# Kernel tuning notes

Hardware: AMD Instinct MI355X
Metric: run time of the kernel (lower is better)

The kernel has to match this reference:

```python
import jax, jax.numpy as jnp
import numpy as np

N = 100000   # nodes
E = 1600000  # edges (before self-loops)
F_IN = 128
H = 64
G = 512      # graphs in batch


def _add_self_loops(edge_index, n):
    loop = jnp.arange(n, dtype=edge_index.dtype)
    src = jnp.concatenate([edge_index[0], loop])
    dst = jnp.concatenate([edge_index[1], loop])
    return src, dst


def _gcn_norm(src, dst, n):
    # PyG GCNConv: deg over targets with self-loops, norm = d^-1/2[src]*d^-1/2[dst]
    deg = jax.ops.segment_sum(jnp.ones_like(dst, dtype=jnp.float32), dst, num_segments=n)
    dinv = jnp.where(deg > 0, jax.lax.rsqrt(deg), 0.0)
    return dinv[src] * dinv[dst]


def _gcn_conv(x, src, dst, norm, W, b):
    xw = x @ W                                # [N, H]
    msg = xw[src] * norm[:, None]             # [E+N, H] gather + scale
    out = jax.ops.segment_sum(msg, dst, num_segments=x.shape[0])
    return out + b


def setup_inputs() -> dict:
    key = jax.random.key(0)
    ks = jax.random.split(key, 9)
    x = jax.random.normal(ks[0], (N, F_IN), dtype=jnp.float32)
    edge_index = jax.random.randint(ks[1], (2, E), 0, N, dtype=jnp.int32)
    batch = jnp.sort(jax.random.randint(ks[2], (N,), 0, G, dtype=jnp.int32))
    s1 = 1.0 / np.sqrt(F_IN)
    s2 = 1.0 / np.sqrt(H)
    W1 = jax.random.uniform(ks[3], (F_IN, H), jnp.float32, -s1, s1)
    b1 = jnp.zeros((H,), jnp.float32)
    W2 = jax.random.uniform(ks[4], (H, H), jnp.float32, -s2, s2)
    b2 = jnp.zeros((H,), jnp.float32)
    Wl = jax.random.uniform(ks[5], (H, 1), jnp.float32, -s2, s2)
    bl = jnp.zeros((1,), jnp.float32)
    return {"x": x, "edge_index": edge_index, "batch": batch,
            "W1": W1, "b1": b1, "W2": W2, "b2": b2, "Wl": Wl, "bl": bl}


def reference(x, edge_index, batch, W1, b1, W2, b2, Wl, bl):
    n = x.shape[0]
    src, dst = _add_self_loops(edge_index, n)
    norm = _gcn_norm(src, dst, n)
    h = jax.nn.relu(_gcn_conv(x, src, dst, norm, W1, b1))
    h = jax.nn.relu(_gcn_conv(h, src, dst, norm, W2, b2))
    # global mean pool over graphs
    sums = jax.ops.segment_sum(h, batch, num_segments=G)          # [G, H]
    cnt = jax.ops.segment_sum(jnp.ones((n,), jnp.float32), batch, num_segments=G)
    pooled = sums / jnp.maximum(cnt, 1.0)[:, None]
    return jax.nn.sigmoid(pooled @ Wl + bl)                        # [G, 1]
```

## Files before the change

kernel.cpp:

```cpp
#include <hip/hip_runtime.h>
#include <hip/hip_bf16.h>
#include <cmath>

#define F_IN 128
#define HDIM 64
#define NPB 128
#define NB1 512
#define CAP 2560

typedef __attribute__((ext_vector_type(8))) short bf16x8;
typedef __attribute__((ext_vector_type(4))) float f32x4;
typedef __attribute__((ext_vector_type(2))) float f32x2;

__device__ __forceinline__ float bf2f(unsigned short u) {
    union { unsigned int i; float f; } v; v.i = ((unsigned int)u) << 16; return v.f;
}
__device__ __forceinline__ unsigned short f2bf(float f) {
    __hip_bfloat16 h = __float2bfloat16(f);
    union { __hip_bfloat16 h; unsigned short u; } c; c.h = h; return c.u;
}
__device__ __forceinline__ unsigned char f2fp8(float f) {
    int p = __builtin_amdgcn_cvt_pk_fp8_f32(f, f, 0, false);
    return (unsigned char)(p & 0xff);
}
__device__ __forceinline__ void fp8x8_acc(uint2 v, float* a) {
    f32x2 f;
    f = __builtin_amdgcn_cvt_pk_f32_fp8(v.x, false); a[0] += f.x; a[1] += f.y;
    f = __builtin_amdgcn_cvt_pk_f32_fp8(v.x, true);  a[2] += f.x; a[3] += f.y;
    f = __builtin_amdgcn_cvt_pk_f32_fp8(v.y, false); a[4] += f.x; a[5] += f.y;
    f = __builtin_amdgcn_cvt_pk_f32_fp8(v.y, true);  a[6] += f.x; a[7] += f.y;
}


__launch_bounds__(256)
__global__ void p0_count(const int* __restrict__ dst, int* __restrict__ blk_cnt,
                         int E, int nbuk, int chunk,
                         const float* __restrict__ W1, const float* __restrict__ W2,
                         unsigned short* __restrict__ w1t, unsigned short* __restrict__ w2t) {
    int tid = threadIdx.x;
    if (blockIdx.x >= NB1) {
        int t = (blockIdx.x - NB1) * 256 + tid;
        if (t < F_IN * 64) {
            int c = t & 63, k = t >> 6;
            w1t[c * F_IN + k] = f2bf(W1[t]);
        } else if (t < F_IN * 64 + HDIM * 64) {
            int u = t - F_IN * 64;
            int c = u & 63, k = u >> 6;
            w2t[c * HDIM + k] = f2bf(W2[u]);
        }
        return;
    }
    __shared__ int hist[1024];
    for (int i = tid; i < nbuk; i += 256) hist[i] = 0;
    __syncthreads();
    int lo = blockIdx.x * chunk;
    int hi = min(E, lo + chunk);
    for (int e = lo + tid; e < hi; e += 256)
        atomicAdd(&hist[dst[e] >> 7], 1);
    __syncthreads();
    for (int i = tid; i < nbuk; i += 256)
        blk_cnt[i * NB1 + blockIdx.x] = hist[i];
}


__launch_bounds__(256)
__global__ void p_scan_blocks(int* __restrict__ blk_cnt, int* __restrict__ bucket_cnt,
                              int nbuk, const int* __restrict__ batch,
                              int* __restrict__ gstart, int n, int G) {
    int tid = threadIdx.x;
    if (blockIdx.x >= nbuk) {
        int g = (blockIdx.x - nbuk) * 256 + tid;
        if (g > G) return;
        int lo = 0, hi = n;
        while (lo < hi) {
            int mid = (lo + hi) >> 1;
            if (batch[mid] < g) lo = mid + 1; else hi = mid;
        }
        gstart[g] = lo;
        return;
    }
    __shared__ int sd[256];
    int b = blockIdx.x;
    int2* row = (int2*)(blk_cnt + (size_t)b * NB1);
    int2 v = row[tid];
    int s0 = v.x, s1 = s0 + v.y;
    sd[tid] = s1;
    __syncthreads();
    for (int off = 1; off < 256; off <<= 1) {
        int a = (tid >= off) ? sd[tid - off] : 0;
        __syncthreads();
        sd[tid] += a;
        __syncthreads();
    }
    int base = sd[tid] - s1;
    row[tid] = make_int2(base, base + s0);
    if (tid == 255) bucket_cnt[b] = sd[255];
}


__launch_bounds__(256)
__global__ void p1_place(const int* __restrict__ src, const int* __restrict__ dst,
                         const int* __restrict__ blk_cnt, int* __restrict__ pairs,
                         int E, int nbuk, int chunk) {
    __shared__ int cur[1024];
    int tid = threadIdx.x;
    for (int i = tid; i < nbuk; i += 256)
        cur[i] = i * CAP + blk_cnt[i * NB1 + blockIdx.x];
    __syncthreads();
    int lo = blockIdx.x * chunk;
    int hi = min(E, lo + chunk);
    for (int e = lo + tid; e < hi; e += 256) {
        int d = dst[e];
        int pos = atomicAdd(&cur[d >> 7], 1);
        pairs[pos] = (src[e] << 7) | (d & 127);
    }
}


__launch_bounds__(256)
__global__ void p2_csr(const int* __restrict__ pairs, const int* __restrict__ bucket_cnt,
                       float* __restrict__ dinv, int* __restrict__ col,
                       int4* __restrict__ slot_hdr, int n) {
    __shared__ int dl[128];
    __shared__ int sc[128];
    __shared__ int cur[128];
    __shared__ int h64[64];
    __shared__ int s64[64];
    int b = blockIdx.x, tid = threadIdx.x;
    int nlo = b << 7;
    int eb = b * CAP;
    int ee = eb + bucket_cnt[b];
    if (tid < 128) dl[tid] = 0;
    if (tid < 64) h64[tid] = 0;
    __syncthreads();
    for (int e = eb + tid; e < ee; e += 256)
        atomicAdd(&dl[pairs[e] & 127], 1);
    __syncthreads();
    int d0 = 0, excl = 0;
    if (tid < 128) {
        d0 = dl[tid];
        sc[tid] = d0;
    }
    __syncthreads();
    for (int off = 1; off < 128; off <<= 1) {
        int a = (tid >= off && tid < 128) ? sc[tid - off] : 0;
        __syncthreads();
        if (tid < 128) sc[tid] += a;
        __syncthreads();
    }
    if (tid < 128) {
        excl = sc[tid] - d0;
        int node = nlo + tid;
        float dv = rsqrtf((float)(d0 + 1));
        if (node < n) dinv[node] = dv;
        cur[tid] = eb + excl;
        int bin = min(d0, 63);
        atomicAdd(&h64[bin], 1);
    }
    __syncthreads();
    if (tid == 0) { int run = 0; for (int i = 0; i < 64; ++i) { s64[i] = run; run += h64[i]; } }
    __syncthreads();
    if (tid < 64) h64[tid] = 0;
    __syncthreads();
    if (tid < 128) {
        int node = nlo + tid;
        int bin = min(d0, 63);
        int pos = s64[bin] + atomicAdd(&h64[bin], 1);
        float dv = rsqrtf((float)(d0 + 1));
        int4 hdr;
        hdr.x = (node < n) ? node : 0x7fffffff;
        hdr.y = eb + excl;
        hdr.z = d0;
        hdr.w = __float_as_int(dv);
        slot_hdr[nlo + pos] = hdr;
    }
    __syncthreads();
    for (int e = eb + tid; e < ee; e += 256) {
        unsigned int v = (unsigned int)pairs[e];
        int p = atomicAdd(&cur[v & 127], 1);
        col[p] = (int)(v >> 7);
    }
}


template <int K>
__launch_bounds__(256)
__global__ void matmul_mfma(const float* __restrict__ X, const unsigned short* __restrict__ Wt,
                            const float* __restrict__ dinv, unsigned char* __restrict__ out,
                            int n) {
    constexpr int KS  = K / 32;
    constexpr int LDX = K + 8;
    __shared__ unsigned short Xs[64 * LDX];
    __shared__ unsigned short Ws[64 * LDX];

    int tid = threadIdx.x;
    int rowbase = blockIdx.x * 64;

    for (int i = tid; i < 64 * (K / 8); i += 256) {
        int r = i / (K / 8), ch = i % (K / 8);
        *(bf16x8*)(Ws + r * LDX + ch * 8) = ((const bf16x8*)Wt)[i];
    }
    {
        const float4* X4 = (const float4*)X;
        for (int i = tid; i < 64 * (K / 4); i += 256) {
            int r = i / (K / 4), k4 = i % (K / 4);
            ushort4 u = { 0, 0, 0, 0 };
            int gr = rowbase + r;
            if (gr < n) {
                float4 v = X4[(size_t)gr * (K / 4) + k4];
                u.x = f2bf(v.x); u.y = f2bf(v.y); u.z = f2bf(v.z); u.w = f2bf(v.w);
            }
            *(ushort4*)(Xs + r * LDX + k4 * 4) = u;
        }
    }
    __syncthreads();

    int wave = tid >> 6, lane = tid & 63;
    int q = lane >> 4, nn = lane & 15;

    f32x4 acc[4] = {{0,0,0,0},{0,0,0,0},{0,0,0,0},{0,0,0,0}};
    int mrow = wave * 16 + nn;
#pragma unroll
    for (int s = 0; s < KS; ++s) {
        bf16x8 af = *(const bf16x8*)(Xs + mrow * LDX + s * 32 + q * 8);
#pragma unroll
        for (int c = 0; c < 4; ++c) {
            bf16x8 bf = *(const bf16x8*)(Ws + (c * 16 + nn) * LDX + s * 32 + q * 8);
            acc[c] = __builtin_amdgcn_mfma_f32_16x16x32_bf16(af, bf, acc[c], 0, 0, 0);
        }
    }

#pragma unroll
    for (int r = 0; r < 4; ++r) {
        int row = rowbase + wave * 16 + q * 4 + r;
        if (row >= n) continue;
        float dv = dinv[row];
#pragma unroll
        for (int c = 0; c < 4; ++c)
            out[(size_t)row * HDIM + c * 16 + nn] = f2fp8(acc[c][r] * dv);
    }
}


__launch_bounds__(256)
__global__ void matmul_mfma_b16(const unsigned short* __restrict__ X,
                                const unsigned short* __restrict__ Wt,
                                const float* __restrict__ dinv, unsigned char* __restrict__ out,
                                int n) {
    constexpr int K = 64, KS = 2, LDX = K + 8;
    __shared__ unsigned short Xs[64 * LDX];
    __shared__ unsigned short Ws[64 * LDX];

    int tid = threadIdx.x;
    int rowbase = blockIdx.x * 64;

    for (int i = tid; i < 64 * (K / 8); i += 256) {
        int r = i / (K / 8), ch = i % (K / 8);
        *(bf16x8*)(Ws + r * LDX + ch * 8) = ((const bf16x8*)Wt)[i];
    }
    for (int i = tid; i < 64 * 8; i += 256) {
        int r = i >> 3, c = i & 7;
        int gr = rowbase + r;
        bf16x8 u;
        if (gr < n) u = ((const bf16x8*)X)[(size_t)gr * 8 + c];
        else { short z[8] = {0,0,0,0,0,0,0,0}; u = *(bf16x8*)z; }
        *(bf16x8*)(Xs + r * LDX + c * 8) = u;
    }
    __syncthreads();

    int wave = tid >> 6, lane = tid & 63;
    int q = lane >> 4, nn = lane & 15;

    f32x4 acc[4] = {{0,0,0,0},{0,0,0,0},{0,0,0,0},{0,0,0,0}};
    int mrow = wave * 16 + nn;
#pragma unroll
    for (int s = 0; s < KS; ++s) {
        bf16x8 af = *(const bf16x8*)(Xs + mrow * LDX + s * 32 + q * 8);
#pragma unroll
        for (int c = 0; c < 4; ++c) {
            bf16x8 bf = *(const bf16x8*)(Ws + (c * 16 + nn) * LDX + s * 32 + q * 8);
            acc[c] = __builtin_amdgcn_mfma_f32_16x16x32_bf16(af, bf, acc[c], 0, 0, 0);
        }
    }

#pragma unroll
    for (int r = 0; r < 4; ++r) {
        int row = rowbase + wave * 16 + q * 4 + r;
        if (row >= n) continue;
        float dv = dinv[row];
#pragma unroll
        for (int c = 0; c < 4; ++c)
            out[(size_t)row * HDIM + c * 16 + nn] = f2fp8(acc[c][r] * dv);
    }
}


__launch_bounds__(256)
__global__ void csr_gather8_fp8(const int4* __restrict__ slot_hdr, const int* __restrict__ col,
                                const uint2* __restrict__ xws, const float* __restrict__ bias,
                                bf16x8* __restrict__ outb, int nslots, int n) {
    int t = blockIdx.x * 256 + threadIdx.x;
    int slot = t >> 3;
    if (slot >= nslots) return;
    int L = t & 7;
    int4 hdr = slot_hdr[slot];
    int node = hdr.x;
    if (node >= n) return;
    int s = hdr.y;
    int end = s + hdr.z;
    float dv = __int_as_float(hdr.w);

    float a[8] = {0, 0, 0, 0, 0, 0, 0, 0};
    fp8x8_acc(xws[(size_t)node * 8 + L], a);

    int e = s;
    for (; e + 8 <= end; e += 8) {
        uint2 v0 = xws[(size_t)col[e + 0] * 8 + L];
        uint2 v1 = xws[(size_t)col[e + 1] * 8 + L];
        uint2 v2 = xws[(size_t)col[e + 2] * 8 + L];
        uint2 v3 = xws[(size_t)col[e + 3] * 8 + L];
        uint2 v4 = xws[(size_t)col[e + 4] * 8 + L];
        uint2 v5 = xws[(size_t)col[e + 5] * 8 + L];
        uint2 v6 = xws[(size_t)col[e + 6] * 8 + L];
        uint2 v7 = xws[(size_t)col[e + 7] * 8 + L];
        fp8x8_acc(v0, a); fp8x8_acc(v1, a); fp8x8_acc(v2, a); fp8x8_acc(v3, a);
        fp8x8_acc(v4, a); fp8x8_acc(v5, a); fp8x8_acc(v6, a); fp8x8_acc(v7, a);
    }
    for (; e + 4 <= end; e += 4) {
        uint2 v0 = xws[(size_t)col[e + 0] * 8 + L];
        uint2 v1 = xws[(size_t)col[e + 1] * 8 + L];
        uint2 v2 = xws[(size_t)col[e + 2] * 8 + L];
        uint2 v3 = xws[(size_t)col[e + 3] * 8 + L];
        fp8x8_acc(v0, a); fp8x8_acc(v1, a); fp8x8_acc(v2, a); fp8x8_acc(v3, a);
    }
    for (; e < end; ++e)
        fp8x8_acc(xws[(size_t)col[e] * 8 + L], a);

    int f0 = L * 8;
    bf16x8 o;
#pragma unroll
    for (int j = 0; j < 8; ++j)
        o[j] = (short)f2bf(fmaxf(fmaf(a[j], dv, bias[f0 + j]), 0.0f));
    outb[(size_t)node * 8 + L] = o;
}


__launch_bounds__(256)
__global__ void pool_head(const unsigned short* __restrict__ h, const int* __restrict__ gstart,
                          const float* __restrict__ Wl, const float* __restrict__ bl,
                          float* __restrict__ out, int G) {
    int g = blockIdx.x;
    int s = gstart[g], e = gstart[g + 1];
    int f  = threadIdx.x & 63;
    int rg = threadIdx.x >> 6;
    float acc = 0.0f;
    for (int i = s + rg; i < e; i += 4)
        acc += bf2f(h[(size_t)i * HDIM + f]);
    __shared__ float red[4][HDIM];
    red[rg][f] = acc;
    __syncthreads();
    if (rg == 0) {
        float v = (red[0][f] + red[1][f]) + (red[2][f] + red[3][f]);
        float c = fmaxf((float)(e - s), 1.0f);
        v = v * Wl[f] * (1.0f / c);
#pragma unroll
        for (int off = 32; off; off >>= 1) v += __shfl_down(v, off, 64);
        if (f == 0) out[g] = 1.0f / (1.0f + expf(-(v + bl[0])));
    }
}


extern "C" void kernel_launch(void* const* d_in, const int* in_sizes, int n_in,
                              void* d_out, int out_size, void* d_ws, size_t ws_size,
                              hipStream_t stream) {
    const float* x   = (const float*)d_in[0];
    const int* ei    = (const int*)d_in[1];
    const int* batch = (const int*)d_in[2];
    const float* W1  = (const float*)d_in[3];
    const float* b1  = (const float*)d_in[4];
    const float* W2  = (const float*)d_in[5];
    const float* b2  = (const float*)d_in[6];
    const float* Wl  = (const float*)d_in[7];
    const float* bl  = (const float*)d_in[8];
    float* out = (float*)d_out;

    const int n = in_sizes[0] / F_IN;
    const int E = in_sizes[1] / 2;
    const int G = out_size;

    const int* srcp = ei;
    const int* dstp = ei + E;

    int nbuk = (n + NPB - 1) / NPB;
    int nslots = nbuk * NPB;

    char* wsb = (char*)d_ws;
    auto alloc = [&](size_t bytes) { char* p = wsb; wsb += (bytes + 255) & ~(size_t)255; return p; };
    float* dinv       = (float*)alloc((size_t)n * 4);
    int4*  slot_hdr   = (int4*)alloc((size_t)nslots * 16);
    int*   bucket_cnt = (int*)alloc(1024 * 4);
    int*   blk_cnt    = (int*)alloc((size_t)nbuk * NB1 * 4);
    int*   pairs      = (int*)alloc((size_t)nbuk * CAP * 4);
    int*   colx       = (int*)alloc((size_t)nbuk * CAP * 4);
    unsigned short* w1t  = (unsigned short*)alloc((size_t)F_IN * HDIM * 2);
    unsigned short* w2t  = (unsigned short*)alloc((size_t)HDIM * HDIM * 2);
    unsigned char*  xws8 = (unsigned char*)alloc((size_t)n * HDIM);
    unsigned short* xh1  = (unsigned short*)alloc((size_t)n * HDIM * 2);
    unsigned short* xh2  = (unsigned short*)alloc((size_t)n * HDIM * 2);
    int*   gstart     = (int*)alloc(((size_t)G + 1) * 4);

    const int TB = 256;
    int gMM  = (n + 63) / 64;
    int chunk = (E + NB1 - 1) / NB1;
    int gG8  = (nslots * 8 + TB - 1) / TB;

    p0_count<<<NB1 + 48, TB, 0, stream>>>(dstp, blk_cnt, E, nbuk, chunk, W1, W2, w1t, w2t);
    p_scan_blocks<<<nbuk + 3, TB, 0, stream>>>(blk_cnt, bucket_cnt, nbuk, batch, gstart, n, G);
    p1_place<<<NB1, TB, 0, stream>>>(srcp, dstp, blk_cnt, pairs, E, nbuk, chunk);
    p2_csr<<<nbuk, TB, 0, stream>>>(pairs, bucket_cnt, dinv, colx, slot_hdr, n);

    matmul_mfma<F_IN><<<gMM, 256, 0, stream>>>(x, w1t, dinv, xws8, n);
    csr_gather8_fp8<<<gG8, TB, 0, stream>>>(slot_hdr, colx, (const uint2*)xws8,
                                            b1, (bf16x8*)xh1, nslots, n);

    matmul_mfma_b16<<<gMM, 256, 0, stream>>>(xh1, w2t, dinv, xws8, n);
    csr_gather8_fp8<<<gG8, TB, 0, stream>>>(slot_hdr, colx, (const uint2*)xws8,
                                            b2, (bf16x8*)xh2, nslots, n);

    pool_head<<<G, 256, 0, stream>>>(xh2, gstart, Wl, bl, out, G);
}
```

Before: 243.4 us.

## Fuse layer-1 matmul into front kernel and apply dinv per edge in gather

The first X@W1 matmul moves into the front count kernel so it no longer waits on degree normalization and runs concurrently with histogram counting. It stores unscaled fp8 XW1, and the first gather kernel multiplies each neighbour by dinv[src] loaded per edge. This removes one kernel launch and a serial dependency, at the cost of an extra random dinv load and multiply per edge in layer 1. W1 is transposed and converted per tile instead of once, and fp8 quantization now happens before scaling.

```diff
diff --git a/kernel.cpp b/kernel.cpp
--- a/kernel.cpp
+++ b/kernel.cpp
@@ -22,6 +22,13 @@
 __device__ __forceinline__ unsigned char f2fp8(float f) {
     int p = __builtin_amdgcn_cvt_pk_fp8_f32(f, f, 0, false);
     return (unsigned char)(p & 0xff);
+}
+__device__ __forceinline__ void fp8x8_fma(uint2 v, float s, float* a) {
+    f32x2 f;
+    f = __builtin_amdgcn_cvt_pk_f32_fp8(v.x, false); a[0] += s * f.x; a[1] += s * f.y;
+    f = __builtin_amdgcn_cvt_pk_f32_fp8(v.x, true);  a[2] += s * f.x; a[3] += s * f.y;
+    f = __builtin_amdgcn_cvt_pk_f32_fp8(v.y, false); a[4] += s * f.x; a[5] += s * f.y;
+    f = __builtin_amdgcn_cvt_pk_f32_fp8(v.y, true);  a[6] += s * f.x; a[7] += s * f.y;
 }
 __device__ __forceinline__ void fp8x8_acc(uint2 v, float* a) {
     f32x2 f;
@@ -33,43 +40,79 @@
 
 
 __launch_bounds__(256)
-__global__ void p0_count(const int* __restrict__ dst, int* __restrict__ blk_cnt,
-                         int E, int nbuk, int chunk,
-                         const float* __restrict__ W1, const float* __restrict__ W2,
-                         unsigned short* __restrict__ w1t, unsigned short* __restrict__ w2t) {
-    int tid = threadIdx.x;
-    if (blockIdx.x >= NB1) {
-        int t = (blockIdx.x - NB1) * 256 + tid;
-        if (t < F_IN * 64) {
-            int c = t & 63, k = t >> 6;
-            w1t[c * F_IN + k] = f2bf(W1[t]);
-        } else if (t < F_IN * 64 + HDIM * 64) {
-            int u = t - F_IN * 64;
-            int c = u & 63, k = u >> 6;
-            w2t[c * HDIM + k] = f2bf(W2[u]);
-        }
+__global__ void fused_front(const int* __restrict__ dst, int* __restrict__ blk_cnt,
+                            int E, int nbuk, int chunk,
+                            const float* __restrict__ X, const float* __restrict__ W1,
+                            unsigned char* __restrict__ xws8, int ntiles, int n,
+                            const float* __restrict__ W2, unsigned short* __restrict__ w2t,
+                            const int* __restrict__ batch, int* __restrict__ gstart, int G) {
+    __shared__ __align__(16) char SMEM[34816];
+    int tid = threadIdx.x, bid = blockIdx.x;
+
+    if (bid < NB1) {
+        int* hist = (int*)SMEM;
+        for (int i = tid; i < nbuk; i += 256) hist[i] = 0;
+        __syncthreads();
+        int lo = bid * chunk, hi = min(E, lo + chunk);
+        for (int e = lo + tid; e < hi; e += 256)
+            atomicAdd(&hist[dst[e] >> 7], 1);
+        __syncthreads();
+        for (int i = tid; i < nbuk; i += 256)
+            blk_cnt[(size_t)i * NB1 + bid] = hist[i];
         return;
     }
-    __shared__ int hist[1024];
-    for (int i = tid; i < nbuk; i += 256) hist[i] = 0;
-    __syncthreads();
-    int lo = blockIdx.x * chunk;
-    int hi = min(E, lo + chunk);
-    for (int e = lo + tid; e < hi; e += 256)
-        atomicAdd(&hist[dst[e] >> 7], 1);
-    __syncthreads();
-    for (int i = tid; i < nbuk; i += 256)
-        blk_cnt[i * NB1 + blockIdx.x] = hist[i];
-}
-
-
-__launch_bounds__(256)
-__global__ void p_scan_blocks(int* __restrict__ blk_cnt, int* __restrict__ bucket_cnt,
-                              int nbuk, const int* __restrict__ batch,
-                              int* __restrict__ gstart, int n, int G) {
-    int tid = threadIdx.x;
-    if (blockIdx.x >= nbuk) {
-        int g = (blockIdx.x - nbuk) * 256 + tid;
+    if (bid < NB1 + ntiles) {
+        constexpr int K = F_IN, KS = K / 32, LDX = K + 8;
+        unsigned short* Xs = (unsigned short*)SMEM;
+        unsigned short* Ws = (unsigned short*)(SMEM + 64 * LDX * 2);
+        int rowbase = (bid - NB1) * 64;
+        for (int i = tid; i < K * 64; i += 256) {
+            int k = i >> 6, c = i & 63;
+            Ws[c * LDX + k] = f2bf(W1[i]);
+        }
+        const float4* X4 = (const float4*)X;
+        for (int i = tid; i < 64 * (K / 4); i += 256) {
+            int r = i / (K / 4), k4 = i % (K / 4);
+            ushort4 u = { 0, 0, 0, 0 };
+            int gr = rowbase + r;
+            if (gr < n) {
+                float4 v = X4[(size_t)gr * (K / 4) + k4];
+                u.x = f2bf(v.x); u.y = f2bf(v.y); u.z = f2bf(v.z); u.w = f2bf(v.w);
+            }
+            *(ushort4*)(Xs + r * LDX + k4 * 4) = u;
+        }
+        __syncthreads();
+        int wave = tid >> 6, lane = tid & 63;
+        int q = lane >> 4, nn = lane & 15;
+        f32x4 acc[4] = {{0,0,0,0},{0,0,0,0},{0,0,0,0},{0,0,0,0}};
+        int mrow = wave * 16 + nn;
+#pragma unroll
+        for (int s = 0; s < KS; ++s) {
+            bf16x8 af = *(const bf16x8*)(Xs + mrow * LDX + s * 32 + q * 8);
+#pragma unroll
+            for (int c = 0; c < 4; ++c) {
+                bf16x8 bf = *(const bf16x8*)(Ws + (c * 16 + nn) * LDX + s * 32 + q * 8);
+                acc[c] = __builtin_amdgcn_mfma_f32_16x16x32_bf16(af, bf, acc[c], 0, 0, 0);
+            }
+        }
+#pragma unroll
+        for (int r = 0; r < 4; ++r) {
+            int row = rowbase + wave * 16 + q * 4 + r;
+            if (row >= n) continue;
+#pragma unroll
+            for (int c = 0; c < 4; ++c)
+                xws8[(size_t)row * HDIM + c * 16 + nn] = f2fp8(acc[c][r]);
+        }
+        return;
+    }
+    if (bid < NB1 + ntiles + 16) {
+        int t = (bid - NB1 - ntiles) * 256 + tid;
+        int c = t & 63, k = t >> 6;
+        w2t[c * HDIM + k] = f2bf(W2[t]);
+        return;
+    }
+    {
+        int g = (bid - NB1 - ntiles - 16) * 256 + tid;
         if (g > G) return;
         int lo = 0, hi = n;
         while (lo < hi) {
@@ -77,10 +120,14 @@
             if (batch[mid] < g) lo = mid + 1; else hi = mid;
         }
         gstart[g] = lo;
-        return;
-    }
+    }
+}
+
+
+__launch_bounds__(256)
+__global__ void p_scan_blocks(int* __restrict__ blk_cnt, int* __restrict__ bucket_cnt) {
     __shared__ int sd[256];
-    int b = blockIdx.x;
+    int b = blockIdx.x, tid = threadIdx.x;
     int2* row = (int2*)(blk_cnt + (size_t)b * NB1);
     int2 v = row[tid];
     int s0 = v.x, s1 = s0 + v.y;
@@ -105,10 +152,9 @@
     __shared__ int cur[1024];
     int tid = threadIdx.x;
     for (int i = tid; i < nbuk; i += 256)
-        cur[i] = i * CAP + blk_cnt[i * NB1 + blockIdx.x];
-    __syncthreads();
-    int lo = blockIdx.x * chunk;
-    int hi = min(E, lo + chunk);
+        cur[i] = i * CAP + blk_cnt[(size_t)i * NB1 + blockIdx.x];
+    __syncthreads();
+    int lo = blockIdx.x * chunk, hi = min(E, lo + chunk);
     for (int e = lo + tid; e < hi; e += 256) {
         int d = dst[e];
         int pos = atomicAdd(&cur[d >> 7], 1);
@@ -137,10 +183,7 @@
         atomicAdd(&dl[pairs[e] & 127], 1);
     __syncthreads();
     int d0 = 0, excl = 0;
-    if (tid < 128) {
-        d0 = dl[tid];
-        sc[tid] = d0;
-    }
+    if (tid < 128) { d0 = dl[tid]; sc[tid] = d0; }
     __syncthreads();
     for (int off = 1; off < 128; off <<= 1) {
         int a = (tid >= off && tid < 128) ? sc[tid - off] : 0;
@@ -154,8 +197,7 @@
         float dv = rsqrtf((float)(d0 + 1));
         if (node < n) dinv[node] = dv;
         cur[tid] = eb + excl;
-        int bin = min(d0, 63);
-        atomicAdd(&h64[bin], 1);
+        atomicAdd(&h64[min(d0, 63)], 1);
     }
     __syncthreads();
     if (tid == 0) { int run = 0; for (int i = 0; i < 64; ++i) { s64[i] = run; run += h64[i]; } }
@@ -166,79 +208,68 @@
         int node = nlo + tid;
         int bin = min(d0, 63);
         int pos = s64[bin] + atomicAdd(&h64[bin], 1);
-        float dv = rsqrtf((float)(d0 + 1));
         int4 hdr;
         hdr.x = (node < n) ? node : 0x7fffffff;
         hdr.y = eb + excl;
         hdr.z = d0;
-        hdr.w = __float_as_int(dv);
+        hdr.w = __float_as_int(rsqrtf((float)(d0 + 1)));
         slot_hdr[nlo + pos] = hdr;
     }
     __syncthreads();
     for (int e = eb + tid; e < ee; e += 256) {
         unsigned int v = (unsigned int)pairs[e];
-        int p = atomicAdd(&cur[v & 127], 1);
-        col[p] = (int)(v >> 7);
-    }
-}
-
-
-template <int K>
-__launch_bounds__(256)
-__global__ void matmul_mfma(const float* __restrict__ X, const unsigned short* __restrict__ Wt,
-                            const float* __restrict__ dinv, unsigned char* __restrict__ out,
-                            int n) {
-    constexpr int KS  = K / 32;
-    constexpr int LDX = K + 8;
-    __shared__ unsigned short Xs[64 * LDX];
-    __shared__ unsigned short Ws[64 * LDX];
-
-    int tid = threadIdx.x;
-    int rowbase = blockIdx.x * 64;
-
-    for (int i = tid; i < 64 * (K / 8); i += 256) {
-        int r = i / (K / 8), ch = i % (K / 8);
-        *(bf16x8*)(Ws + r * LDX + ch * 8) = ((const bf16x8*)Wt)[i];
-    }
-    {
-        const float4* X4 = (const float4*)X;
-        for (int i = tid; i < 64 * (K / 4); i += 256) {
-            int r = i / (K / 4), k4 = i % (K / 4);
-            ushort4 u = { 0, 0, 0, 0 };
-            int gr = rowbase + r;
-            if (gr < n) {
-                float4 v = X4[(size_t)gr * (K / 4) + k4];
-                u.x = f2bf(v.x); u.y = f2bf(v.y); u.z = f2bf(v.z); u.w = f2bf(v.w);
-            }
-            *(ushort4*)(Xs + r * LDX + k4 * 4) = u;
-        }
-    }
-    __syncthreads();
-
-    int wave = tid >> 6, lane = tid & 63;
-    int q = lane >> 4, nn = lane & 15;
-
-    f32x4 acc[4] = {{0,0,0,0},{0,0,0,0},{0,0,0,0},{0,0,0,0}};
-    int mrow = wave * 16 + nn;
-#pragma unroll
-    for (int s = 0; s < KS; ++s) {
-        bf16x8 af = *(const bf16x8*)(Xs + mrow * LDX + s * 32 + q * 8);
-#pragma unroll
-        for (int c = 0; c < 4; ++c) {
-            bf16x8 bf = *(const bf16x8*)(Ws + (c * 16 + nn) * LDX + s * 32 + q * 8);
-            acc[c] = __builtin_amdgcn_mfma_f32_16x16x32_bf16(af, bf, acc[c], 0, 0, 0);
-        }
-    }
-
-#pragma unroll
-    for (int r = 0; r < 4; ++r) {
-        int row = rowbase + wave * 16 + q * 4 + r;
-        if (row >= n) continue;
-        float dv = dinv[row];
-#pragma unroll
-        for (int c = 0; c < 4; ++c)
-            out[(size_t)row * HDIM + c * 16 + nn] = f2fp8(acc[c][r] * dv);
-    }
+        int pos = atomicAdd(&cur[v & 127], 1);
+        col[pos] = (int)(v >> 7);
+    }
+}
+
+
+__launch_bounds__(256)
+__global__ void csr_gather8_fp8d(const int4* __restrict__ slot_hdr, const int* __restrict__ col,
+                                 const float* __restrict__ dinv, const uint2* __restrict__ xws,
+                                 const float* __restrict__ bias, bf16x8* __restrict__ outb,
+                                 int nslots, int n) {
+    int t = blockIdx.x * 256 + threadIdx.x;
+    int slot = t >> 3;
+    if (slot >= nslots) return;
+    int L = t & 7;
+    int4 hdr = slot_hdr[slot];
+    int node = hdr.x;
+    if (node >= n) return;
+    int s = hdr.y, end = s + hdr.z;
+    float dv = __int_as_float(hdr.w);
+
+    float a[8] = {0, 0, 0, 0, 0, 0, 0, 0};
+    fp8x8_fma(xws[(size_t)node * 8 + L], dv, a);
+
+    int e = s;
+    for (; e + 8 <= end; e += 8) {
+        int c0 = col[e + 0], c1 = col[e + 1], c2 = col[e + 2], c3 = col[e + 3];
+        int c4 = col[e + 4], c5 = col[e + 5], c6 = col[e + 6], c7 = col[e + 7];
+        float d0 = dinv[c0], d1 = dinv[c1], d2 = dinv[c2], d3 = dinv[c3];
+        float d4 = dinv[c4], d5 = dinv[c5], d6 = dinv[c6], d7 = dinv[c7];
+        uint2 v0 = xws[(size_t)c0 * 8 + L];
+        uint2 v1 = xws[(size_t)c1 * 8 + L];
+        uint2 v2 = xws[(size_t)c2 * 8 + L];
+        uint2 v3 = xws[(size_t)c3 * 8 + L];
+        uint2 v4 = xws[(size_t)c4 * 8 + L];
+        uint2 v5 = xws[(size_t)c5 * 8 + L];
+        uint2 v6 = xws[(size_t)c6 * 8 + L];
+        uint2 v7 = xws[(size_t)c7 * 8 + L];
+        fp8x8_fma(v0, d0, a); fp8x8_fma(v1, d1, a); fp8x8_fma(v2, d2, a); fp8x8_fma(v3, d3, a);
+        fp8x8_fma(v4, d4, a); fp8x8_fma(v5, d5, a); fp8x8_fma(v6, d6, a); fp8x8_fma(v7, d7, a);
+    }
+    for (; e < end; ++e) {
+        int c = col[e];
+        fp8x8_fma(xws[(size_t)c * 8 + L], dinv[c], a);
+    }
+
+    int f0 = L * 8;
+    bf16x8 o;
+#pragma unroll
+    for (int j = 0; j < 8; ++j)
+        o[j] = (short)f2bf(fmaxf(fmaf(a[j], dv, bias[f0 + j]), 0.0f));
+    outb[(size_t)node * 8 + L] = o;
 }
 
 
@@ -250,10 +281,8 @@
     constexpr int K = 64, KS = 2, LDX = K + 8;
     __shared__ unsigned short Xs[64 * LDX];
     __shared__ unsigned short Ws[64 * LDX];
-
     int tid = threadIdx.x;
     int rowbase = blockIdx.x * 64;
-
     for (int i = tid; i < 64 * (K / 8); i += 256) {
         int r = i / (K / 8), ch = i % (K / 8);
         *(bf16x8*)(Ws + r * LDX + ch * 8) = ((const bf16x8*)Wt)[i];
@@ -267,10 +296,8 @@
         *(bf16x8*)(Xs + r * LDX + c * 8) = u;
     }
     __syncthreads();
-
     int wave = tid >> 6, lane = tid & 63;
     int q = lane >> 4, nn = lane & 15;
-
     f32x4 acc[4] = {{0,0,0,0},{0,0,0,0},{0,0,0,0},{0,0,0,0}};
     int mrow = wave * 16 + nn;
 #pragma unroll
@@ -282,7 +309,6 @@
             acc[c] = __builtin_amdgcn_mfma_f32_16x16x32_bf16(af, bf, acc[c], 0, 0, 0);
         }
     }
-
 #pragma unroll
     for (int r = 0; r < 4; ++r) {
         int row = rowbase + wave * 16 + q * 4 + r;
@@ -306,8 +332,7 @@
     int4 hdr = slot_hdr[slot];
     int node = hdr.x;
     if (node >= n) return;
-    int s = hdr.y;
-    int end = s + hdr.z;
+    int s = hdr.y, end = s + hdr.z;
     float dv = __int_as_float(hdr.w);
 
     float a[8] = {0, 0, 0, 0, 0, 0, 0, 0};
@@ -325,13 +350,6 @@
         uint2 v7 = xws[(size_t)col[e + 7] * 8 + L];
         fp8x8_acc(v0, a); fp8x8_acc(v1, a); fp8x8_acc(v2, a); fp8x8_acc(v3, a);
         fp8x8_acc(v4, a); fp8x8_acc(v5, a); fp8x8_acc(v6, a); fp8x8_acc(v7, a);
-    }
-    for (; e + 4 <= end; e += 4) {
-        uint2 v0 = xws[(size_t)col[e + 0] * 8 + L];
-        uint2 v1 = xws[(size_t)col[e + 1] * 8 + L];
-        uint2 v2 = xws[(size_t)col[e + 2] * 8 + L];
-        uint2 v3 = xws[(size_t)col[e + 3] * 8 + L];
-        fp8x8_acc(v0, a); fp8x8_acc(v1, a); fp8x8_acc(v2, a); fp8x8_acc(v3, a);
     }
     for (; e < end; ++e)
         fp8x8_acc(xws[(size_t)col[e] * 8 + L], a);
@@ -402,7 +420,6 @@
     int*   blk_cnt    = (int*)alloc((size_t)nbuk * NB1 * 4);
     int*   pairs      = (int*)alloc((size_t)nbuk * CAP * 4);
     int*   colx       = (int*)alloc((size_t)nbuk * CAP * 4);
-    unsigned short* w1t  = (unsigned short*)alloc((size_t)F_IN * HDIM * 2);
     unsigned short* w2t  = (unsigned short*)alloc((size_t)HDIM * HDIM * 2);
     unsigned char*  xws8 = (unsigned char*)alloc((size_t)n * HDIM);
     unsigned short* xh1  = (unsigned short*)alloc((size_t)n * HDIM * 2);
@@ -413,19 +430,18 @@
     int gMM  = (n + 63) / 64;
     int chunk = (E + NB1 - 1) / NB1;
     int gG8  = (nslots * 8 + TB - 1) / TB;
-
-    p0_count<<<NB1 + 48, TB, 0, stream>>>(dstp, blk_cnt, E, nbuk, chunk, W1, W2, w1t, w2t);
-    p_scan_blocks<<<nbuk + 3, TB, 0, stream>>>(blk_cnt, bucket_cnt, nbuk, batch, gstart, n, G);
+    int gFront = NB1 + gMM + 16 + 3;
+
+    fused_front<<<gFront, TB, 0, stream>>>(dstp, blk_cnt, E, nbuk, chunk,
+                                           x, W1, xws8, gMM, n, W2, w2t, batch, gstart, G);
+    p_scan_blocks<<<nbuk, TB, 0, stream>>>(blk_cnt, bucket_cnt);
     p1_place<<<NB1, TB, 0, stream>>>(srcp, dstp, blk_cnt, pairs, E, nbuk, chunk);
     p2_csr<<<nbuk, TB, 0, stream>>>(pairs, bucket_cnt, dinv, colx, slot_hdr, n);
 
-    matmul_mfma<F_IN><<<gMM, 256, 0, stream>>>(x, w1t, dinv, xws8, n);
-    csr_gather8_fp8<<<gG8, TB, 0, stream>>>(slot_hdr, colx, (const uint2*)xws8,
-                                            b1, (bf16x8*)xh1, nslots, n);
-
-    matmul_mfma_b16<<<gMM, 256, 0, stream>>>(xh1, w2t, dinv, xws8, n);
+    csr_gather8_fp8d<<<gG8, TB, 0, stream>>>(slot_hdr, colx, dinv, (const uint2*)xws8,
+                                             b1, (bf16x8*)xh1, nslots, n);
+    matmul_mfma_b16<<<gMM, TB, 0, stream>>>(xh1, w2t, dinv, xws8, n);
     csr_gather8_fp8<<<gG8, TB, 0, stream>>>(slot_hdr, colx, (const uint2*)xws8,
                                             b2, (bf16x8*)xh2, nslots, n);
-
-    pool_head<<<G, 256, 0, stream>>>(xh2, gstart, Wl, bl, out, G);
-}
+    pool_head<<<G, TB, 0, stream>>>(xh2, gstart, Wl, bl, out, G);
+}
```

New measurement: 246.5 us. About the same (+1.2%).

## Fuse layer-1 CSR gather with layer-2 MFMA matmul into one kernel

Applied to the files above, without the earlier changes.

Merges the first aggregation (gather over CSR neighbours, bias, ReLU) with the second layer's 64x64 bf16 MFMA transform. Each block gathers 32 slots into shared memory, multiplies them by W2 and writes fp8 scaled output straight to node-indexed rows. This removes the bf16 intermediate write and re-read of h1 and one kernel launch. In exchange each block now reloads W2 into LDS, output stores are scattered because slots are degree-sorted, and the smaller 32-slot tile may reduce MFMA efficiency. The 4-wide remainder loop in the gather is also dropped, and there are minor cosmetic edits.

```diff
diff --git a/kernel.cpp b/kernel.cpp
--- a/kernel.cpp
+++ b/kernel.cpp
@@ -53,13 +53,12 @@
     __shared__ int hist[1024];
     for (int i = tid; i < nbuk; i += 256) hist[i] = 0;
     __syncthreads();
-    int lo = blockIdx.x * chunk;
-    int hi = min(E, lo + chunk);
+    int lo = blockIdx.x * chunk, hi = min(E, lo + chunk);
     for (int e = lo + tid; e < hi; e += 256)
         atomicAdd(&hist[dst[e] >> 7], 1);
     __syncthreads();
     for (int i = tid; i < nbuk; i += 256)
-        blk_cnt[i * NB1 + blockIdx.x] = hist[i];
+        blk_cnt[(size_t)i * NB1 + blockIdx.x] = hist[i];
 }
 
 
@@ -105,10 +104,9 @@
     __shared__ int cur[1024];
     int tid = threadIdx.x;
     for (int i = tid; i < nbuk; i += 256)
-        cur[i] = i * CAP + blk_cnt[i * NB1 + blockIdx.x];
-    __syncthreads();
-    int lo = blockIdx.x * chunk;
-    int hi = min(E, lo + chunk);
+        cur[i] = i * CAP + blk_cnt[(size_t)i * NB1 + blockIdx.x];
+    __syncthreads();
+    int lo = blockIdx.x * chunk, hi = min(E, lo + chunk);
     for (int e = lo + tid; e < hi; e += 256) {
         int d = dst[e];
         int pos = atomicAdd(&cur[d >> 7], 1);
@@ -137,10 +135,7 @@
         atomicAdd(&dl[pairs[e] & 127], 1);
     __syncthreads();
     int d0 = 0, excl = 0;
-    if (tid < 128) {
-        d0 = dl[tid];
-        sc[tid] = d0;
-    }
+    if (tid < 128) { d0 = dl[tid]; sc[tid] = d0; }
     __syncthreads();
     for (int off = 1; off < 128; off <<= 1) {
         int a = (tid >= off && tid < 128) ? sc[tid - off] : 0;
@@ -154,8 +149,7 @@
         float dv = rsqrtf((float)(d0 + 1));
         if (node < n) dinv[node] = dv;
         cur[tid] = eb + excl;
-        int bin = min(d0, 63);
-        atomicAdd(&h64[bin], 1);
+        atomicAdd(&h64[min(d0, 63)], 1);
     }
     __syncthreads();
     if (tid == 0) { int run = 0; for (int i = 0; i < 64; ++i) { s64[i] = run; run += h64[i]; } }
@@ -166,19 +160,18 @@
         int node = nlo + tid;
         int bin = min(d0, 63);
         int pos = s64[bin] + atomicAdd(&h64[bin], 1);
-        float dv = rsqrtf((float)(d0 + 1));
         int4 hdr;
         hdr.x = (node < n) ? node : 0x7fffffff;
         hdr.y = eb + excl;
         hdr.z = d0;
-        hdr.w = __float_as_int(dv);
+        hdr.w = __float_as_int(rsqrtf((float)(d0 + 1)));
         slot_hdr[nlo + pos] = hdr;
     }
     __syncthreads();
     for (int e = eb + tid; e < ee; e += 256) {
         unsigned int v = (unsigned int)pairs[e];
-        int p = atomicAdd(&cur[v & 127], 1);
-        col[p] = (int)(v >> 7);
+        int pos = atomicAdd(&cur[v & 127], 1);
+        col[pos] = (int)(v >> 7);
     }
 }
 
@@ -192,10 +185,8 @@
     constexpr int LDX = K + 8;
     __shared__ unsigned short Xs[64 * LDX];
     __shared__ unsigned short Ws[64 * LDX];
-
     int tid = threadIdx.x;
     int rowbase = blockIdx.x * 64;
-
     for (int i = tid; i < 64 * (K / 8); i += 256) {
         int r = i / (K / 8), ch = i % (K / 8);
         *(bf16x8*)(Ws + r * LDX + ch * 8) = ((const bf16x8*)Wt)[i];
@@ -214,10 +205,8 @@
         }
     }
     __syncthreads();
-
     int wave = tid >> 6, lane = tid & 63;
     int q = lane >> 4, nn = lane & 15;
-
     f32x4 acc[4] = {{0,0,0,0},{0,0,0,0},{0,0,0,0},{0,0,0,0}};
     int mrow = wave * 16 + nn;
 #pragma unroll
@@ -229,7 +218,6 @@
             acc[c] = __builtin_amdgcn_mfma_f32_16x16x32_bf16(af, bf, acc[c], 0, 0, 0);
         }
     }
-
 #pragma unroll
     for (int r = 0; r < 4; ++r) {
         int row = rowbase + wave * 16 + q * 4 + r;
@@ -243,54 +231,91 @@
 
 
 __launch_bounds__(256)
-__global__ void matmul_mfma_b16(const unsigned short* __restrict__ X,
-                                const unsigned short* __restrict__ Wt,
-                                const float* __restrict__ dinv, unsigned char* __restrict__ out,
-                                int n) {
-    constexpr int K = 64, KS = 2, LDX = K + 8;
-    __shared__ unsigned short Xs[64 * LDX];
-    __shared__ unsigned short Ws[64 * LDX];
+__global__ void gather1_mm2(const int4* __restrict__ slot_hdr, const int* __restrict__ col,
+                            const uint2* __restrict__ xws, const float* __restrict__ bias,
+                            const unsigned short* __restrict__ w2t,
+                            unsigned char* __restrict__ out8, int nslots, int n) {
+    __shared__ unsigned short Hs[32 * 72];
+    __shared__ unsigned short Ws[64 * 72];
+    __shared__ int   snode[32];
+    __shared__ float sdinv[32];
 
     int tid = threadIdx.x;
-    int rowbase = blockIdx.x * 64;
-
-    for (int i = tid; i < 64 * (K / 8); i += 256) {
-        int r = i / (K / 8), ch = i % (K / 8);
-        *(bf16x8*)(Ws + r * LDX + ch * 8) = ((const bf16x8*)Wt)[i];
-    }
+    int ls = tid >> 3;
+    int L  = tid & 7;
+    int slot = blockIdx.x * 32 + ls;
+
     for (int i = tid; i < 64 * 8; i += 256) {
-        int r = i >> 3, c = i & 7;
-        int gr = rowbase + r;
-        bf16x8 u;
-        if (gr < n) u = ((const bf16x8*)X)[(size_t)gr * 8 + c];
-        else { short z[8] = {0,0,0,0,0,0,0,0}; u = *(bf16x8*)z; }
-        *(bf16x8*)(Xs + r * LDX + c * 8) = u;
+        int r = i >> 3, ch = i & 7;
+        *(bf16x8*)(Ws + r * 72 + ch * 8) = ((const bf16x8*)w2t)[i];
+    }
+
+    int node = 0x7fffffff;
+    float dv = 0.0f;
+    float a[8] = {0, 0, 0, 0, 0, 0, 0, 0};
+    if (slot < nslots) {
+        int4 hdr = slot_hdr[slot];
+        node = hdr.x;
+        if (node < n) {
+            int s = hdr.y, end = s + hdr.z;
+            dv = __int_as_float(hdr.w);
+            fp8x8_acc(xws[(size_t)node * 8 + L], a);
+            int e = s;
+            for (; e + 8 <= end; e += 8) {
+                uint2 v0 = xws[(size_t)col[e + 0] * 8 + L];
+                uint2 v1 = xws[(size_t)col[e + 1] * 8 + L];
+                uint2 v2 = xws[(size_t)col[e + 2] * 8 + L];
+                uint2 v3 = xws[(size_t)col[e + 3] * 8 + L];
+                uint2 v4 = xws[(size_t)col[e + 4] * 8 + L];
+                uint2 v5 = xws[(size_t)col[e + 5] * 8 + L];
+                uint2 v6 = xws[(size_t)col[e + 6] * 8 + L];
+                uint2 v7 = xws[(size_t)col[e + 7] * 8 + L];
+                fp8x8_acc(v0, a); fp8x8_acc(v1, a); fp8x8_acc(v2, a); fp8x8_acc(v3, a);
+                fp8x8_acc(v4, a); fp8x8_acc(v5, a); fp8x8_acc(v6, a); fp8x8_acc(v7, a);
+            }
+            for (; e < end; ++e)
+                fp8x8_acc(xws[(size_t)col[e] * 8 + L], a);
+        }
+    }
+    if (L == 0) { snode[ls] = node; sdinv[ls] = dv; }
+    {
+        int f0 = L * 8;
+        bf16x8 o;
+        if (node < n) {
+#pragma unroll
+            for (int j = 0; j < 8; ++j)
+                o[j] = (short)f2bf(fmaxf(fmaf(a[j], dv, bias[f0 + j]), 0.0f));
+        } else {
+            short z[8] = {0,0,0,0,0,0,0,0};
+            o = *(bf16x8*)z;
+        }
+        *(bf16x8*)(Hs + ls * 72 + L * 8) = o;
     }
     __syncthreads();
 
     int wave = tid >> 6, lane = tid & 63;
     int q = lane >> 4, nn = lane & 15;
-
-    f32x4 acc[4] = {{0,0,0,0},{0,0,0,0},{0,0,0,0},{0,0,0,0}};
-    int mrow = wave * 16 + nn;
-#pragma unroll
-    for (int s = 0; s < KS; ++s) {
-        bf16x8 af = *(const bf16x8*)(Xs + mrow * LDX + s * 32 + q * 8);
-#pragma unroll
-        for (int c = 0; c < 4; ++c) {
-            bf16x8 bf = *(const bf16x8*)(Ws + (c * 16 + nn) * LDX + s * 32 + q * 8);
-            acc[c] = __builtin_amdgcn_mfma_f32_16x16x32_bf16(af, bf, acc[c], 0, 0, 0);
-        }
-    }
-
+    int mt  = wave & 1;
+    int nt0 = (wave >> 1) * 2;
+    f32x4 acc[2] = {{0,0,0,0},{0,0,0,0}};
+#pragma unroll
+    for (int s = 0; s < 2; ++s) {
+        bf16x8 af = *(const bf16x8*)(Hs + (mt * 16 + nn) * 72 + s * 32 + q * 8);
+#pragma unroll
+        for (int t = 0; t < 2; ++t) {
+            bf16x8 bf = *(const bf16x8*)(Ws + ((nt0 + t) * 16 + nn) * 72 + s * 32 + q * 8);
+            acc[t] = __builtin_amdgcn_mfma_f32_16x16x32_bf16(af, bf, acc[t], 0, 0, 0);
+        }
+    }
 #pragma unroll
     for (int r = 0; r < 4; ++r) {
-        int row = rowbase + wave * 16 + q * 4 + r;
-        if (row >= n) continue;
-        float dv = dinv[row];
-#pragma unroll
-        for (int c = 0; c < 4; ++c)
-            out[(size_t)row * HDIM + c * 16 + nn] = f2fp8(acc[c][r] * dv);
+        int lslot = mt * 16 + q * 4 + r;
+        int nd = snode[lslot];
+        if (nd >= n) continue;
+        float dvr = sdinv[lslot];
+#pragma unroll
+        for (int t = 0; t < 2; ++t)
+            out8[(size_t)nd * HDIM + (nt0 + t) * 16 + nn] = f2fp8(acc[t][r] * dvr);
     }
 }
 
@@ -306,13 +331,11 @@
     int4 hdr = slot_hdr[slot];
     int node = hdr.x;
     if (node >= n) return;
-    int s = hdr.y;
-    int end = s + hdr.z;
+    int s = hdr.y, end = s + hdr.z;
     float dv = __int_as_float(hdr.w);
 
     float a[8] = {0, 0, 0, 0, 0, 0, 0, 0};
     fp8x8_acc(xws[(size_t)node * 8 + L], a);
-
     int e = s;
     for (; e + 8 <= end; e += 8) {
         uint2 v0 = xws[(size_t)col[e + 0] * 8 + L];
@@ -325,13 +348,6 @@
         uint2 v7 = xws[(size_t)col[e + 7] * 8 + L];
         fp8x8_acc(v0, a); fp8x8_acc(v1, a); fp8x8_acc(v2, a); fp8x8_acc(v3, a);
         fp8x8_acc(v4, a); fp8x8_acc(v5, a); fp8x8_acc(v6, a); fp8x8_acc(v7, a);
-    }
-    for (; e + 4 <= end; e += 4) {
-        uint2 v0 = xws[(size_t)col[e + 0] * 8 + L];
-        uint2 v1 = xws[(size_t)col[e + 1] * 8 + L];
-        uint2 v2 = xws[(size_t)col[e + 2] * 8 + L];
-        uint2 v3 = xws[(size_t)col[e + 3] * 8 + L];
-        fp8x8_acc(v0, a); fp8x8_acc(v1, a); fp8x8_acc(v2, a); fp8x8_acc(v3, a);
     }
     for (; e < end; ++e)
         fp8x8_acc(xws[(size_t)col[e] * 8 + L], a);
@@ -405,7 +421,7 @@
     unsigned short* w1t  = (unsigned short*)alloc((size_t)F_IN * HDIM * 2);
     unsigned short* w2t  = (unsigned short*)alloc((size_t)HDIM * HDIM * 2);
     unsigned char*  xws8 = (unsigned char*)alloc((size_t)n * HDIM);
-    unsigned short* xh1  = (unsigned short*)alloc((size_t)n * HDIM * 2);
+    unsigned char*  xws8b= (unsigned char*)alloc((size_t)n * HDIM);
     unsigned short* xh2  = (unsigned short*)alloc((size_t)n * HDIM * 2);
     int*   gstart     = (int*)alloc(((size_t)G + 1) * 4);
 
@@ -413,19 +429,17 @@
     int gMM  = (n + 63) / 64;
     int chunk = (E + NB1 - 1) / NB1;
     int gG8  = (nslots * 8 + TB - 1) / TB;
+    int gS   = (nslots + 31) / 32;
 
     p0_count<<<NB1 + 48, TB, 0, stream>>>(dstp, blk_cnt, E, nbuk, chunk, W1, W2, w1t, w2t);
     p_scan_blocks<<<nbuk + 3, TB, 0, stream>>>(blk_cnt, bucket_cnt, nbuk, batch, gstart, n, G);
     p1_place<<<NB1, TB, 0, stream>>>(srcp, dstp, blk_cnt, pairs, E, nbuk, chunk);
     p2_csr<<<nbuk, TB, 0, stream>>>(pairs, bucket_cnt, dinv, colx, slot_hdr, n);
 
-    matmul_mfma<F_IN><<<gMM, 256, 0, stream>>>(x, w1t, dinv, xws8, n);
-    csr_gather8_fp8<<<gG8, TB, 0, stream>>>(slot_hdr, colx, (const uint2*)xws8,
-                                            b1, (bf16x8*)xh1, nslots, n);
-
-    matmul_mfma_b16<<<gMM, 256, 0, stream>>>(xh1, w2t, dinv, xws8, n);
-    csr_gather8_fp8<<<gG8, TB, 0, stream>>>(slot_hdr, colx, (const uint2*)xws8,
+    matmul_mfma<F_IN><<<gMM, TB, 0, stream>>>(x, w1t, dinv, xws8, n);
+    gather1_mm2<<<gS, TB, 0, stream>>>(slot_hdr, colx, (const uint2*)xws8,
+                                       b1, w2t, xws8b, nslots, n);
+    csr_gather8_fp8<<<gG8, TB, 0, stream>>>(slot_hdr, colx, (const uint2*)xws8b,
                                             b2, (bf16x8*)xh2, nslots, n);
-
-    pool_head<<<G, 256, 0, stream>>>(xh2, gstart, Wl, bl, out, G);
-}
+    pool_head<<<G, TB, 0, stream>>>(xh2, gstart, Wl, bl, out, G);
+}
```

After: 236.4 us. 2.9% less time.
